# Kernel tuning notes

Measured on AMD Instinct MI355X. Metric: run time of the kernel, lower is better.

Reference implementation:

```python
import jax, jax.numpy as jnp
import numpy as np

LAMB = 0.01
DISTILL = 1.0
NUM_CLASSES = 10


def _reverse_seq(x, lens):
    # TF reverse_sequence semantics: reverse first `lens[i]` steps of row i.
    T = x.shape[1]
    t = jnp.arange(T)[None, :]
    idx = jnp.where(t < lens[:, None], lens[:, None] - 1 - t, t)
    return jnp.take_along_axis(x, idx[:, :, None], axis=1)


def _run_gru(x, lens, Wg, bg, Wc, bc):
    # TF GRUCell: r,z = sigmoid([x,h]Wg + bg); c = tanh([x, r*h]Wc + bc); h' = z*h + (1-z)*c
    # dynamic_rnn: past sequence_length, state is frozen and output is zero.
    N, T, _ = x.shape
    H = Wc.shape[1]
    h0 = jnp.zeros((N, H), x.dtype)

    def step(h, inp):
        x_t, t = inp
        xh = jnp.concatenate([x_t, h], axis=-1)
        rz = jax.nn.sigmoid(xh @ Wg + bg)
        r, z = jnp.split(rz, 2, axis=-1)
        c = jnp.tanh(jnp.concatenate([x_t, r * h], axis=-1) @ Wc + bc)
        h_new = z * h + (1.0 - z) * c
        valid = (t < lens)[:, None]
        return jnp.where(valid, h_new, h), jnp.where(valid, h_new, 0.0)

    _, outs = jax.lax.scan(step, h0, (x.transpose(1, 0, 2), jnp.arange(T)))
    return outs.transpose(1, 0, 2)  # [N, T, H]


def _bigru(x, lens, pfw, pbw):
    fw = _run_gru(x, lens, *pfw)
    bw = _reverse_seq(_run_gru(_reverse_seq(x, lens), lens, *pbw), lens)
    return jnp.concatenate([fw, bw], axis=-1)  # [N, T, 2H]


def _attention(out, Wa, ba, u):
    # additive attention: tanh projection -> score with context vector -> softmax -> weighted sum
    proj = jnp.tanh(out @ Wa + ba)                      # [N, T, A]
    score = jnp.squeeze(proj @ u, -1) / DISTILL         # [N, T]
    att = jax.nn.softmax(score, axis=1)
    vec = jnp.einsum('nt,nth->nh', att, out)            # [N, 2H]
    return vec, att


def setup_inputs() -> dict:
    key = jax.random.key(0)
    ks = jax.random.split(key, 40)
    B, D, S, E, H, C = 64, 40, 50, 200, 128, 10
    rn = lambda k, shp, s=0.1: (jax.random.normal(k, shp) * s).astype(jnp.float32)
    inp = {}
    inp['X_sentence'] = jax.random.normal(ks[0], (B, D, S, E), jnp.float32)
    inp['y'] = jax.random.randint(ks[1], (B,), 0, C).astype(jnp.int32)
    inp['sentence_length'] = jax.random.randint(ks[2], (B * D,), 1, S + 1).astype(jnp.int32)
    inp['document_length'] = jax.random.randint(ks[3], (B,), 1, D + 1).astype(jnp.int32)
    inp['dropout'] = 0
    inp['is_training'] = 0
    i = [4]
    def nxt():
        k = ks[i[0]]; i[0] += 1; return k
    for lvl, din in (('l', E), ('h', 2 * H)):
        for d in ('f', 'b'):
            inp['wg' + d + '_' + lvl] = rn(nxt(), (din + H, 2 * H))
            inp['bg' + d + '_' + lvl] = jnp.ones((2 * H,), jnp.float32)  # TF GRU gate bias init = 1.0
            inp['wc' + d + '_' + lvl] = rn(nxt(), (din + H, H))
            inp['bc' + d + '_' + lvl] = jnp.zeros((H,), jnp.float32)
        inp['wa_' + lvl] = rn(nxt(), (2 * H, H))
        inp['ba_' + lvl] = jnp.zeros((H,), jnp.float32)
    inp['uw'] = rn(nxt(), (H, 1), 1.0)  # random_normal stddev=1.0 as in source
    inp['us'] = rn(nxt(), (H, 1), 1.0)
    inp['wp'] = rn(nxt(), (2 * H, C))
    inp['bp'] = jnp.zeros((C,), jnp.float32)
    return inp


def reference(X_sentence, y, sentence_length, document_length, dropout, is_training,
              wgf_l, bgf_l, wcf_l, bcf_l, wgb_l, bgb_l, wcb_l, bcb_l, wa_l, ba_l,
              wgf_h, bgf_h, wcf_h, bcf_h, wgb_h, bgb_h, wcb_h, bcb_h, wa_h, ba_h,
              uw, us, wp, bp):
    # inference mode (is_training=False -> tf.layers.dropout is identity)
    B, D, S, E = X_sentence.shape
    x = X_sentence.reshape(B * D, S, E)
    # word level
    low = _bigru(x, sentence_length, (wgf_l, bgf_l, wcf_l, bcf_l), (wgb_l, bgb_l, wcb_l, bcb_l))
    sent_vec, att_low = _attention(low, wa_l, ba_l, uw)            # [B*D, 2H], [B*D, S]
    sent = sent_vec.reshape(B, D, -1)
    # sentence level
    high = _bigru(sent, document_length, (wgf_h, bgf_h, wcf_h, bcf_h), (wgb_h, bgb_h, wcb_h, bcb_h))
    doc_vec, att_high = _attention(high, wa_h, ba_h, us)           # [B, 2H], [B, D]
    logits = doc_vec @ wp + bp                                     # [B, C]
    logp = jax.nn.log_softmax(logits, axis=-1)
    loss = -jnp.mean(jnp.take_along_axis(logp, y[:, None], axis=1))
    # regularizer exactly as in source (note h kernel counted twice, h bias omitted)
    loss = loss + LAMB * (jnp.sum(wa_l ** 2) + jnp.sum(ba_l ** 2)
                          + 2.0 * jnp.sum(wa_h ** 2)
                          + jnp.sum(uw ** 2) + jnp.sum(us ** 2))
    predict = jnp.argmax(logits, axis=1).astype(jnp.int32)
    accuracy = jnp.mean((y == predict).astype(jnp.float32))
    return (loss, predict, accuracy, att_low, att_high)
```

## Files before the change

### kernel.cpp

```cpp
#include <hip/hip_runtime.h>
#include <hip/hip_bf16.h>


typedef __attribute__((ext_vector_type(8))) short short8;
typedef __attribute__((ext_vector_type(4))) float f32x4;

__device__ __forceinline__ float fsigmoid(float x) { return 1.f / (1.f + __expf(-x)); }
__device__ __forceinline__ float ftanh(float x)    { float e = __expf(2.f * x); return 1.f - 2.f / (e + 1.f); }

__device__ __forceinline__ unsigned short f2bf(float x) {
    unsigned int u = __builtin_bit_cast(unsigned int, x);
    u += 0x7fffu + ((u >> 16) & 1u);
    return (unsigned short)(u >> 16);
}
__device__ __forceinline__ float bf2f(unsigned short h) {
    unsigned int u = ((unsigned int)h) << 16;
    return __builtin_bit_cast(float, u);
}
__device__ __forceinline__ uint4 pack8(const unsigned short* v) {
    uint4 r;
    r.x = (unsigned int)v[0] | ((unsigned int)v[1] << 16);
    r.y = (unsigned int)v[2] | ((unsigned int)v[3] << 16);
    r.z = (unsigned int)v[4] | ((unsigned int)v[5] << 16);
    r.w = (unsigned int)v[6] | ((unsigned int)v[7] << 16);
    return r;
}
__device__ __forceinline__ void cvt8(const float* v, short8& hi, short8& lo) {
    unsigned short h[8], l[8];
#pragma unroll
    for (int j = 0; j < 8; ++j) {
        unsigned short hh = f2bf(v[j]);
        h[j] = hh;
        l[j] = f2bf(v[j] - bf2f(hh));
    }
    uint4 uh = pack8(h), ul = pack8(l);
    hi = __builtin_bit_cast(short8, uh);
    lo = __builtin_bit_cast(short8, ul);
}

__global__ __launch_bounds__(256) void pack_weights(
    const float* __restrict__ wg_f, const float* __restrict__ bg_f,
    const float* __restrict__ wc_f, const float* __restrict__ bc_f,
    const float* __restrict__ wg_b, const float* __restrict__ bg_b,
    const float* __restrict__ wc_b, const float* __restrict__ bc_b,
    float* __restrict__ W, float* __restrict__ bias, int E)
{
    int idx = blockIdx.x * 256 + threadIdx.x;
    if (idx < 768) {
        int c = idx; float v;
        if (c < 256) v = bg_f[c];
        else if (c < 384) v = bc_f[c - 256];
        else if (c < 640) v = bg_b[c - 384];
        else v = bc_b[c - 640];
        bias[c] = v;
    }
    if (idx >= E * 768) return;
    int k = idx / 768, c = idx - k * 768;
    float v;
    if (c < 256) v = wg_f[k * 256 + c];
    else if (c < 384) v = wc_f[k * 128 + (c - 256)];
    else if (c < 640) v = wg_b[k * 256 + (c - 384)];
    else v = wc_b[k * 128 + (c - 640)];
    W[idx] = v;
}

__global__ __launch_bounds__(256) void pack_a_frag(
    const float* __restrict__ src, uint4* __restrict__ dstH, uint4* __restrict__ dstL,
    int Mr16, int KC, int Ks)
{
    int idx = blockIdx.x * 256 + threadIdx.x;
    if (idx >= Mr16 * KC * 64) return;
    int lane = idx & 63;
    int g = idx >> 6;
    int mb = g / KC, kc = g - mb * KC;
    int m = lane & 15, quad = lane >> 4;
    int row = mb * 16 + m;
    int k0 = kc * 32 + quad * 8;
    const float* s = src + (size_t)row * Ks;
    unsigned short hi[8], lo[8];
#pragma unroll
    for (int j = 0; j < 8; ++j) {
        float x = (k0 + j < Ks) ? s[k0 + j] : 0.f;
        unsigned short h = f2bf(x);
        hi[j] = h;
        lo[j] = f2bf(x - bf2f(h));
    }
    dstH[idx] = pack8(hi);
    dstL[idx] = pack8(lo);
}

__global__ __launch_bounds__(256) void pack_w_frag(
    const float* __restrict__ src, uint4* __restrict__ dstH, uint4* __restrict__ dstL,
    int N16, int KC, int Ks, int N)
{
    int idx = blockIdx.x * 256 + threadIdx.x;
    if (idx >= N16 * KC * 64) return;
    int lane = idx & 63;
    int g = idx >> 6;
    int nb = g / KC, kc = g - nb * KC;
    int m = lane & 15, quad = lane >> 4;
    int n = nb * 16 + m;
    int k0 = kc * 32 + quad * 8;
    unsigned short hi[8], lo[8];
#pragma unroll
    for (int j = 0; j < 8; ++j) {
        float x = (k0 + j < Ks) ? src[(size_t)(k0 + j) * N + n] : 0.f;
        unsigned short h = f2bf(x);
        hi[j] = h;
        lo[j] = f2bf(x - bf2f(h));
    }
    dstH[idx] = pack8(hi);
    dstL[idx] = pack8(lo);
}

__global__ __launch_bounds__(256) void pack_rec(
    const float* __restrict__ wgf, const float* __restrict__ wgb,
    const float* __restrict__ wcf, const float* __restrict__ wcb,
    uint4* __restrict__ RgH, uint4* __restrict__ RgL,
    uint4* __restrict__ RcH, uint4* __restrict__ RcL)
{
    int sel = blockIdx.y;
    const float* src; uint4 *dH, *dL; int N16, N;
    if (sel == 0)      { src = wgf; dH = RgH;        dL = RgL;        N16 = 16; N = 256; }
    else if (sel == 1) { src = wgb; dH = RgH + 4096; dL = RgL + 4096; N16 = 16; N = 256; }
    else if (sel == 2) { src = wcf; dH = RcH;        dL = RcL;        N16 = 8;  N = 128; }
    else               { src = wcb; dH = RcH + 2048; dL = RcL + 2048; N16 = 8;  N = 128; }
    int idx = blockIdx.x * 256 + threadIdx.x;
    if (idx >= N16 * 4 * 64) return;
    int lane = idx & 63;
    int g = idx >> 6;
    int nb = g / 4, kc = g - nb * 4;
    int m = lane & 15, quad = lane >> 4;
    int n = nb * 16 + m;
    int k0 = kc * 32 + quad * 8;
    unsigned short hi[8], lo[8];
#pragma unroll
    for (int j = 0; j < 8; ++j) {
        float x = src[(size_t)(k0 + j) * N + n];
        unsigned short h = f2bf(x);
        hi[j] = h;
        lo[j] = f2bf(x - bf2f(h));
    }
    dH[idx] = pack8(hi);
    dL[idx] = pack8(lo);
}

__global__ __launch_bounds__(256) void mfma_gemm(
    const uint4* __restrict__ Ah, const uint4* __restrict__ Al,
    const uint4* __restrict__ Bh, const uint4* __restrict__ Bl,
    const float* __restrict__ bias, float* __restrict__ C,
    int KC, int ldc, int act)
{
    int tid = threadIdx.x;
    int lane = tid & 63;
    int w = tid >> 6;
    int wm = w >> 1, wn = w & 1;
    int quad = lane >> 4, m = lane & 15;
    int bm = blockIdx.x, bn = blockIdx.y;
    f32x4 acc[4][4];
#pragma unroll
    for (int i = 0; i < 4; ++i)
#pragma unroll
        for (int j = 0; j < 4; ++j) acc[i][j] = (f32x4){0.f, 0.f, 0.f, 0.f};

    size_t aBase[4], bBase[4];
#pragma unroll
    for (int i = 0; i < 4; ++i) {
        aBase[i] = ((size_t)(bm * 8 + wm * 4 + i) * KC) * 64 + quad * 16 + m;
        bBase[i] = ((size_t)(bn * 8 + wn * 4 + i) * KC) * 64 + quad * 16 + m;
    }
    for (int kc = 0; kc < KC; ++kc) {
        short8 ah[4], al[4], bh[4], bl[4];
#pragma unroll
        for (int i = 0; i < 4; ++i) {
            ah[i] = __builtin_bit_cast(short8, Ah[aBase[i]]);
            al[i] = __builtin_bit_cast(short8, Al[aBase[i]]);
            bh[i] = __builtin_bit_cast(short8, Bh[bBase[i]]);
            bl[i] = __builtin_bit_cast(short8, Bl[bBase[i]]);
            aBase[i] += 64; bBase[i] += 64;
        }
#pragma unroll
        for (int i = 0; i < 4; ++i)
#pragma unroll
            for (int j = 0; j < 4; ++j) {
                acc[i][j] = __builtin_amdgcn_mfma_f32_16x16x32_bf16(ah[i], bh[j], acc[i][j], 0, 0, 0);
                acc[i][j] = __builtin_amdgcn_mfma_f32_16x16x32_bf16(ah[i], bl[j], acc[i][j], 0, 0, 0);
                acc[i][j] = __builtin_amdgcn_mfma_f32_16x16x32_bf16(al[i], bh[j], acc[i][j], 0, 0, 0);
            }
    }
#pragma unroll
    for (int i = 0; i < 4; ++i) {
        int row0 = bm * 128 + wm * 64 + i * 16 + quad * 4;
#pragma unroll
        for (int j = 0; j < 4; ++j) {
            int col = bn * 128 + wn * 64 + j * 16 + m;
            float b = bias[col];
#pragma unroll
            for (int r = 0; r < 4; ++r) {
                float v = acc[i][j][r] + b;
                if (act) v = ftanh(v);
                C[(size_t)(row0 + r) * ldc + col] = v;
            }
        }
    }
}

__global__ __launch_bounds__(256) void bigru_mfma(
    const float* __restrict__ G,
    const uint4* __restrict__ WgH, const uint4* __restrict__ WgL,
    const uint4* __restrict__ WcH, const uint4* __restrict__ WcL,
    const int* __restrict__ lens,
    float* __restrict__ outbuf,
    int rowOff, int T)
{
    __shared__ float hs[16][132];
    __shared__ float zs[16][132];
    __shared__ uint4 hfH[4][64], hfL[4][64];
    __shared__ uint4 rfH[4][64], rfL[4][64];
    __shared__ int Ls[16];

    int tid = threadIdx.x;
    int dir = blockIdx.x & 1;
    int rg0 = (blockIdx.x >> 1) * 16;
    int lane = tid & 63, w = tid >> 6;
    int quad = lane >> 4, mc = lane & 15;
    for (int i = tid; i < 16 * 132; i += 256) { (&hs[0][0])[i] = 0.f; }
    for (int i = tid; i < 256; i += 256) { hfH[0][i] = (uint4){0,0,0,0}; hfL[0][i] = (uint4){0,0,0,0}; }
    if (tid < 16) Ls[tid] = lens[rowOff + rg0 + tid];
    __syncthreads();
    const int goff = dir * 384;
    unsigned short* hfHu = (unsigned short*)hfH;
    unsigned short* hfLu = (unsigned short*)hfL;
    unsigned short* rfHu = (unsigned short*)rfH;
    unsigned short* rfLu = (unsigned short*)rfL;

    for (int t = 0; t < T; ++t) {
        int Lr[4], tir[4];
#pragma unroll
        for (int r = 0; r < 4; ++r) {
            int L = Ls[quad * 4 + r];
            Lr[r] = L;
            tir[r] = dir ? ((t < L) ? (L - 1 - t) : t) : t;
        }
        float gG[4][4], gC[2][4];
#pragma unroll
        for (int r = 0; r < 4; ++r) {
            const float* gbase = &G[((size_t)(rg0 + quad * 4 + r) * T + tir[r]) * 768 + goff];
#pragma unroll
            for (int i = 0; i < 4; ++i) gG[i][r] = gbase[(w * 4 + i) * 16 + mc];
#pragma unroll
            for (int i = 0; i < 2; ++i) gC[i][r] = gbase[256 + (w * 2 + i) * 16 + mc];
        }
        f32x4 ga[4];
#pragma unroll
        for (int i = 0; i < 4; ++i) ga[i] = (f32x4){0.f, 0.f, 0.f, 0.f};
#pragma unroll
        for (int kc = 0; kc < 4; ++kc) {
            short8 ah = __builtin_bit_cast(short8, hfH[kc][lane]);
            short8 al = __builtin_bit_cast(short8, hfL[kc][lane]);
#pragma unroll
            for (int i = 0; i < 4; ++i) {
                size_t idx = (((size_t)(dir * 16 + w * 4 + i) * 4 + kc) << 6) + lane;
                short8 bh = __builtin_bit_cast(short8, WgH[idx]);
                short8 bl = __builtin_bit_cast(short8, WgL[idx]);
                ga[i] = __builtin_amdgcn_mfma_f32_16x16x32_bf16(ah, bh, ga[i], 0, 0, 0);
                ga[i] = __builtin_amdgcn_mfma_f32_16x16x32_bf16(ah, bl, ga[i], 0, 0, 0);
                ga[i] = __builtin_amdgcn_mfma_f32_16x16x32_bf16(al, bh, ga[i], 0, 0, 0);
            }
        }
#pragma unroll
        for (int i = 0; i < 4; ++i) {
            int n = (w * 4 + i) * 16 + mc;
#pragma unroll
            for (int r = 0; r < 4; ++r) {
                int m = quad * 4 + r;
                float s = fsigmoid(ga[i][r] + gG[i][r]);
                if (n < 128) {
                    float rh = s * hs[m][n];
                    unsigned short hi = f2bf(rh);
                    int fi = ((((n >> 5) * 64) + (((n >> 3) & 3) * 16) + m) << 3) + (n & 7);
                    rfHu[fi] = hi;
                    rfLu[fi] = f2bf(rh - bf2f(hi));
                } else {
                    zs[m][n - 128] = s;
                }
            }
        }
        __syncthreads();
        f32x4 ca[2];
#pragma unroll
        for (int i = 0; i < 2; ++i) ca[i] = (f32x4){0.f, 0.f, 0.f, 0.f};
#pragma unroll
        for (int kc = 0; kc < 4; ++kc) {
            short8 ar = __builtin_bit_cast(short8, rfH[kc][lane]);
            short8 al = __builtin_bit_cast(short8, rfL[kc][lane]);
#pragma unroll
            for (int i = 0; i < 2; ++i) {
                size_t idx = (((size_t)(dir * 8 + w * 2 + i) * 4 + kc) << 6) + lane;
                short8 bh = __builtin_bit_cast(short8, WcH[idx]);
                short8 bl = __builtin_bit_cast(short8, WcL[idx]);
                ca[i] = __builtin_amdgcn_mfma_f32_16x16x32_bf16(ar, bh, ca[i], 0, 0, 0);
                ca[i] = __builtin_amdgcn_mfma_f32_16x16x32_bf16(ar, bl, ca[i], 0, 0, 0);
                ca[i] = __builtin_amdgcn_mfma_f32_16x16x32_bf16(al, bh, ca[i], 0, 0, 0);
            }
        }
#pragma unroll
        for (int i = 0; i < 2; ++i) {
            int n = (w * 2 + i) * 16 + mc;
            int fi0 = ((((n >> 5) * 64) + (((n >> 3) & 3) * 16)) << 3) + (n & 7);
#pragma unroll
            for (int r = 0; r < 4; ++r) {
                int m = quad * 4 + r;
                bool valid = (t < Lr[r]);
                float cd = ftanh(ca[i][r] + gC[i][r]);
                float z = zs[m][n];
                float h = hs[m][n];
                float hn = z * h + (1.f - z) * cd;
                float ov = valid ? hn : 0.f;
                if (valid) {
                    hs[m][n] = hn;
                    unsigned short hi = f2bf(hn);
                    int fi = fi0 + (m << 3);
                    hfHu[fi] = hi;
                    hfLu[fi] = f2bf(hn - bf2f(hi));
                }
                outbuf[((size_t)(rg0 + m) * T + tir[r]) * 256 + dir * 128 + n] = ov;
            }
        }
        __syncthreads();
    }
}

__global__ __launch_bounds__(256) void attn_fused(
    const float* __restrict__ outv,
    const uint4* __restrict__ WaH, const uint4* __restrict__ WaL,
    const float* __restrict__ ba, const float* __restrict__ u,
    float* __restrict__ att_out,
    float* __restrict__ vec,
    int T, int attRowOff)
{
    __shared__ float lowS[50][260];
    __shared__ float scoreS[64];
    __shared__ float attS[64];
    int n = blockIdx.x;
    int tid = threadIdx.x;
    int lane = tid & 63, w = tid >> 6;
    int quad = lane >> 4, mc = lane & 15;

    const float4* src4 = (const float4*)(outv + (size_t)n * T * 256);
    for (int idx = tid; idx < T * 64; idx += 256) {
        int row = idx >> 6, c4 = idx & 63;
        float4 v = src4[idx];
        *(float4*)&lowS[row][c4 * 4] = v;
    }
    __syncthreads();

    f32x4 acc[8];
#pragma unroll
    for (int j = 0; j < 8; ++j) acc[j] = (f32x4){0.f, 0.f, 0.f, 0.f};
    int rowA = w * 16 + mc;
    bool rowValid = rowA < T;
#pragma unroll
    for (int kc = 0; kc < 8; ++kc) {
        float v[8];
        if (rowValid) {
            const float* p = &lowS[rowA][kc * 32 + quad * 8];
#pragma unroll
            for (int j = 0; j < 8; ++j) v[j] = p[j];
        } else {
#pragma unroll
            for (int j = 0; j < 8; ++j) v[j] = 0.f;
        }
        short8 ah, al;
        cvt8(v, ah, al);
#pragma unroll
        for (int nt = 0; nt < 8; ++nt) {
            size_t idx = (((size_t)nt * 8 + kc) << 6) + lane;
            short8 bh = __builtin_bit_cast(short8, WaH[idx]);
            short8 bl = __builtin_bit_cast(short8, WaL[idx]);
            acc[nt] = __builtin_amdgcn_mfma_f32_16x16x32_bf16(ah, bh, acc[nt], 0, 0, 0);
            acc[nt] = __builtin_amdgcn_mfma_f32_16x16x32_bf16(ah, bl, acc[nt], 0, 0, 0);
            acc[nt] = __builtin_amdgcn_mfma_f32_16x16x32_bf16(al, bh, acc[nt], 0, 0, 0);
        }
    }
    float sc[4] = {0.f, 0.f, 0.f, 0.f};
#pragma unroll
    for (int nt = 0; nt < 8; ++nt) {
        int col = nt * 16 + mc;
        float bb = ba[col], uu = u[col];
#pragma unroll
        for (int r = 0; r < 4; ++r)
            sc[r] += ftanh(acc[nt][r] + bb) * uu;
    }
#pragma unroll
    for (int off = 1; off < 16; off <<= 1) {
#pragma unroll
        for (int r = 0; r < 4; ++r) sc[r] += __shfl_xor(sc[r], off);
    }
    if (mc == 0) {
#pragma unroll
        for (int r = 0; r < 4; ++r) scoreS[w * 16 + quad * 4 + r] = sc[r];
    }
    __syncthreads();
    if (w == 0) {
        float s = (lane < T) ? scoreS[lane] : -3.402823466e38f;
        float m = s;
#pragma unroll
        for (int off = 1; off < 64; off <<= 1) m = fmaxf(m, __shfl_xor(m, off));
        float e = (lane < T) ? __expf(s - m) : 0.f;
        float sum = e;
#pragma unroll
        for (int off = 1; off < 64; off <<= 1) sum += __shfl_xor(sum, off);
        float att = e / sum;
        attS[lane] = att;
        if (lane < T) att_out[(size_t)(attRowOff + n) * T + lane] = att;
    }
    __syncthreads();
    float a = 0.f;
    for (int t = 0; t < T; ++t) a += attS[t] * lowS[t][tid];
    vec[(size_t)n * 256 + tid] = a;
}

__global__ __launch_bounds__(256) void head_kernel(
    const float* __restrict__ dvec, const float* __restrict__ wp, const float* __restrict__ bp,
    const int* __restrict__ y,
    const float* __restrict__ wa_l, const float* __restrict__ ba_l, const float* __restrict__ wa_h,
    const float* __restrict__ uw, const float* __restrict__ us,
    float* __restrict__ out)
{
    __shared__ float lg[64][10];
    __shared__ float red[256];
    int tid = threadIdx.x;
    for (int idx = tid; idx < 640; idx += 256) {
        int r = idx / 10, c = idx % 10;
        float a = bp[c];
        const float* dv = dvec + r * 256;
        for (int k = 0; k < 256; ++k) a += dv[k] * wp[k * 10 + c];
        lg[r][c] = a;
    }
    __syncthreads();
    float lossv = 0.f, corr = 0.f;
    if (tid < 64) {
        float m = lg[tid][0]; int arg = 0;
        for (int c = 1; c < 10; ++c) if (lg[tid][c] > m) { m = lg[tid][c]; arg = c; }
        float se = 0.f;
        for (int c = 0; c < 10; ++c) se += __expf(lg[tid][c] - m);
        float lse = m + __logf(se);
        int yy = y[tid];
        lossv = -(lg[tid][yy] - lse);
        corr = (yy == arg) ? 1.f : 0.f;
        out[1 + tid] = (float)arg;
    }
    float rs = 0.f;
    for (int i = tid; i < 32768; i += 256) {
        float v = wa_l[i]; rs += v * v;
        float w = wa_h[i]; rs += 2.f * w * w;
    }
    if (tid < 128) {
        float v1 = ba_l[tid], v2 = uw[tid], v3 = us[tid];
        rs += v1 * v1 + v2 * v2 + v3 * v3;
    }
    red[tid] = lossv; __syncthreads();
    for (int o = 128; o > 0; o >>= 1) { if (tid < o) red[tid] += red[tid + o]; __syncthreads(); }
    float totLoss = red[0]; __syncthreads();
    red[tid] = corr; __syncthreads();
    for (int o = 128; o > 0; o >>= 1) { if (tid < o) red[tid] += red[tid + o]; __syncthreads(); }
    float totCorr = red[0]; __syncthreads();
    red[tid] = rs; __syncthreads();
    for (int o = 128; o > 0; o >>= 1) { if (tid < o) red[tid] += red[tid + o]; __syncthreads(); }
    float totReg = red[0];
    if (tid == 0) {
        out[0] = totLoss / 64.f + 0.01f * totReg;
        out[65] = totCorr / 64.f;
    }
}

extern "C" void kernel_launch(void* const* d_in, const int* in_sizes, int n_in,
                              void* d_out, int out_size, void* d_ws, size_t ws_size,
                              hipStream_t stream)
{
    const float* X    = (const float*)d_in[0];
    const int*   y    = (const int*)d_in[1];
    const int*   slen = (const int*)d_in[2];
    const int*   dlen = (const int*)d_in[3];
    const float* wgf_l = (const float*)d_in[6];
    const float* bgf_l = (const float*)d_in[7];
    const float* wcf_l = (const float*)d_in[8];
    const float* bcf_l = (const float*)d_in[9];
    const float* wgb_l = (const float*)d_in[10];
    const float* bgb_l = (const float*)d_in[11];
    const float* wcb_l = (const float*)d_in[12];
    const float* bcb_l = (const float*)d_in[13];
    const float* wa_l  = (const float*)d_in[14];
    const float* ba_l  = (const float*)d_in[15];
    const float* wgf_h = (const float*)d_in[16];
    const float* bgf_h = (const float*)d_in[17];
    const float* wcf_h = (const float*)d_in[18];
    const float* bcf_h = (const float*)d_in[19];
    const float* wgb_h = (const float*)d_in[20];
    const float* bgb_h = (const float*)d_in[21];
    const float* wcb_h = (const float*)d_in[22];
    const float* bcb_h = (const float*)d_in[23];
    const float* wa_h  = (const float*)d_in[24];
    const float* ba_h  = (const float*)d_in[25];
    const float* uw    = (const float*)d_in[26];
    const float* us    = (const float*)d_in[27];
    const float* wp    = (const float*)d_in[28];
    const float* bp    = (const float*)d_in[29];
    float* out = (float*)d_out;

    int NCH = 1;
    while (NCH < 8) {
        size_t M1t = 128000ull / NCH;
        size_t needB = (M1t * 1248ull + 5200000ull) * 4ull;
        if (needB <= ws_size) break;
        NCH *= 2;
    }
    size_t nRows = 2560 / NCH;
    size_t M1 = nRows * 50;

    float* G1     = (float*)d_ws;
    float* low    = G1 + M1 * 768;
    float* AXf    = low + M1 * 256;
    float* sent   = AXf + M1 * 224;
    float* Gs     = sent + 655360;
    float* high   = Gs + 1966080;
    float* dvec   = high + 655360;
    float* pSf    = dvec + 16384;
    float* WpackL = pSf + 655360;
    float* biasL  = WpackL + 153600;
    float* WLf    = biasL + 768;
    float* WpackH = WLf + 172032;
    float* biasH  = WpackH + 196608;
    float* WHf    = biasH + 768;
    float* WaLf   = WHf + 196608;
    float* WaHf   = WaLf + 32768;
    float* RgLf   = WaHf + 32768;
    float* RcLf   = RgLf + 65536;
    float* RgHf   = RcLf + 32768;
    float* RcHf   = RgHf + 65536;

    uint4* AXh = (uint4*)AXf;           uint4* AXl = (uint4*)(AXf + M1 * 112);
    uint4* pSh = (uint4*)pSf;           uint4* pSl = (uint4*)(pSf + 327680);
    uint4* WLh = (uint4*)WLf;           uint4* WLl = (uint4*)(WLf + 86016);
    uint4* WHh = (uint4*)WHf;           uint4* WHl = (uint4*)(WHf + 98304);
    uint4* WaLh = (uint4*)WaLf;         uint4* WaLl = (uint4*)(WaLf + 16384);
    uint4* WaHh = (uint4*)WaHf;         uint4* WaHl = (uint4*)(WaHf + 16384);
    uint4* RgLH = (uint4*)RgLf;         uint4* RgLL = (uint4*)(RgLf + 32768);
    uint4* RcLH = (uint4*)RcLf;         uint4* RcLL = (uint4*)(RcLf + 16384);
    uint4* RgHH = (uint4*)RgHf;         uint4* RgHL = (uint4*)(RgHf + 32768);
    uint4* RcHH = (uint4*)RcHf;         uint4* RcHL = (uint4*)(RcHf + 16384);

    pack_weights<<<600, 256, 0, stream>>>(wgf_l, bgf_l, wcf_l, bcf_l, wgb_l, bgb_l, wcb_l, bcb_l,
                                          WpackL, biasL, 200);
    pack_weights<<<768, 256, 0, stream>>>(wgf_h, bgf_h, wcf_h, bcf_h, wgb_h, bgb_h, wcb_h, bcb_h,
                                          WpackH, biasH, 256);
    pack_w_frag<<<84, 256, 0, stream>>>(WpackL, WLh, WLl, 48, 7, 200, 768);
    pack_w_frag<<<96, 256, 0, stream>>>(WpackH, WHh, WHl, 48, 8, 256, 768);
    pack_w_frag<<<16, 256, 0, stream>>>(wa_l, WaLh, WaLl, 8, 8, 256, 128);
    pack_w_frag<<<16, 256, 0, stream>>>(wa_h, WaHh, WaHl, 8, 8, 256, 128);
    pack_rec<<<dim3(16, 4), 256, 0, stream>>>(wgf_l + 200 * 256, wgb_l + 200 * 256,
                                              wcf_l + 200 * 128, wcb_l + 200 * 128,
                                              RgLH, RgLL, RcLH, RcLL);
    pack_rec<<<dim3(16, 4), 256, 0, stream>>>(wgf_h + 256 * 256, wgb_h + 256 * 256,
                                              wcf_h + 256 * 128, wcb_h + 256 * 128,
                                              RgHH, RgHL, RcHH, RcHL);

    for (int c = 0; c < NCH; ++c) {
        const float* Xc = X + (size_t)c * nRows * 50 * 200;
        int Mr16 = (int)(M1 / 16);
        pack_a_frag<<<(Mr16 * 7 * 64 + 255) / 256, 256, 0, stream>>>(Xc, AXh, AXl, Mr16, 7, 200);
        mfma_gemm<<<dim3((int)(M1 / 128), 6), 256, 0, stream>>>(AXh, AXl, WLh, WLl, biasL, G1, 7, 768, 0);
        bigru_mfma<<<(int)(nRows / 16) * 2, 256, 0, stream>>>(G1, RgLH, RgLL, RcLH, RcLL,
                                                              slen, low, (int)(c * nRows), 50);
        attn_fused<<<(int)nRows, 256, 0, stream>>>(low, WaLh, WaLl, ba_l, uw,
                                                   out + 66, sent + (size_t)c * nRows * 256, 50, (int)(c * nRows));
    }
    pack_a_frag<<<(160 * 8 * 64 + 255) / 256, 256, 0, stream>>>(sent, pSh, pSl, 160, 8, 256);
    mfma_gemm<<<dim3(20, 6), 256, 0, stream>>>(pSh, pSl, WHh, WHl, biasH, Gs, 8, 768, 0);
    bigru_mfma<<<8, 256, 0, stream>>>(Gs, RgHH, RgHL, RcHH, RcHL, dlen, high, 0, 40);
    attn_fused<<<64, 256, 0, stream>>>(high, WaHh, WaHl, ba_h, us, out + 128066, dvec, 40, 0);
    head_kernel<<<1, 256, 0, stream>>>(dvec, wp, bp, y, wa_l, ba_l, wa_h, uw, us, out);
}
```

Before: 1.237 ms.

## Use two-wave GRU blocks with double-buffered LDS prefetch of gate inputs

Rewrites the recurrent GRU kernel to run with 128 threads (two waves) instead of four. Each wave now does twice the MFMA tiles, and the gate split is reassigned so wave 0 computes r and wave 1 computes z. The next timestep's precomputed gate inputs are prefetched from global memory into registers and staged into a double-buffered LDS area, which takes global-load latency off the sequential critical path. The fp32 hidden-state copy is dropped and h is rebuilt from the bf16 hi/lo split. The tradeoffs are fewer waves per block, less per-step parallelism, and a large LDS footprint that may limit occupancy.

```diff
diff --git a/kernel.cpp b/kernel.cpp
--- a/kernel.cpp
+++ b/kernel.cpp
@@ -205,7 +205,7 @@
     }
 }
 
-__global__ __launch_bounds__(256) void bigru_mfma(
+__global__ __launch_bounds__(128) void bigru_wave(
     const float* __restrict__ G,
     const uint4* __restrict__ WgH, const uint4* __restrict__ WgL,
     const uint4* __restrict__ WcH, const uint4* __restrict__ WcL,
@@ -213,54 +213,82 @@
     float* __restrict__ outbuf,
     int rowOff, int T)
 {
-    __shared__ float hs[16][132];
-    __shared__ float zs[16][132];
+    __shared__ float Gb[2][6400];
     __shared__ uint4 hfH[4][64], hfL[4][64];
     __shared__ uint4 rfH[4][64], rfL[4][64];
-    __shared__ int Ls[16];
-
-    int tid = threadIdx.x;
-    int dir = blockIdx.x & 1;
-    int rg0 = (blockIdx.x >> 1) * 16;
-    int lane = tid & 63, w = tid >> 6;
-    int quad = lane >> 4, mc = lane & 15;
-    for (int i = tid; i < 16 * 132; i += 256) { (&hs[0][0])[i] = 0.f; }
-    for (int i = tid; i < 256; i += 256) { hfH[0][i] = (uint4){0,0,0,0}; hfL[0][i] = (uint4){0,0,0,0}; }
-    if (tid < 16) Ls[tid] = lens[rowOff + rg0 + tid];
-    __syncthreads();
-    const int goff = dir * 384;
+    __shared__ float zs[16][130];
+
+    const int tid = threadIdx.x;
+    const int lane = tid & 63, w = tid >> 6;
+    const int quad = lane >> 4, mc = lane & 15;
+    const int dir = blockIdx.x & 1;
+    const int rg0 = (blockIdx.x >> 1) * 16;
+
     unsigned short* hfHu = (unsigned short*)hfH;
     unsigned short* hfLu = (unsigned short*)hfL;
     unsigned short* rfHu = (unsigned short*)rfH;
     unsigned short* rfLu = (unsigned short*)rfL;
 
+    for (int i = tid; i < 256; i += 128) {
+        hfH[0][i] = (uint4){0, 0, 0, 0};
+        hfL[0][i] = (uint4){0, 0, 0, 0};
+    }
+    int Lr[4];
+#pragma unroll
+    for (int r = 0; r < 4; ++r) Lr[r] = lens[rowOff + rg0 + quad * 4 + r];
+
+    const int k0 = w * 13;
+    const int nk = w ? 12 : 13;
+    int meta[13];
+    float4 sreg[13];
+    const char* Gblk = (const char*)(G + ((size_t)rg0 * T * 768 + dir * 384));
+#pragma unroll
+    for (int k = 0; k < 13; ++k) {
+        if (k < nk) {
+            int g = (k0 + k) * 64 + lane;
+            int m = g / 97; if (m > 15) m = 15;
+            int c4 = g - m * 97; if (c4 > 96) c4 = 96;
+            int L = lens[rowOff + rg0 + m];
+            meta[k] = (m * T * 3072 + c4 * 16) | (L << 26);
+        }
+    }
+#pragma unroll
+    for (int k = 0; k < 13; ++k) if (k < nk) {
+        int off = meta[k] & 0x03FFFFFF;
+        int L = (int)(((unsigned int)meta[k]) >> 26);
+        int sel = (dir && 0 < L) ? (L - 1) : 0;
+        sreg[k] = *(const float4*)(Gblk + (size_t)off + (size_t)sel * 3072);
+    }
+    {
+        float4* dst = (float4*)&Gb[0][0];
+#pragma unroll
+        for (int k = 0; k < 13; ++k) if (k < nk) dst[(k0 + k) * 64 + lane] = sreg[k];
+    }
+    __syncthreads();
+
     for (int t = 0; t < T; ++t) {
-        int Lr[4], tir[4];
-#pragma unroll
-        for (int r = 0; r < 4; ++r) {
-            int L = Ls[quad * 4 + r];
-            Lr[r] = L;
-            tir[r] = dir ? ((t < L) ? (L - 1 - t) : t) : t;
-        }
-        float gG[4][4], gC[2][4];
-#pragma unroll
-        for (int r = 0; r < 4; ++r) {
-            const float* gbase = &G[((size_t)(rg0 + quad * 4 + r) * T + tir[r]) * 768 + goff];
-#pragma unroll
-            for (int i = 0; i < 4; ++i) gG[i][r] = gbase[(w * 4 + i) * 16 + mc];
-#pragma unroll
-            for (int i = 0; i < 2; ++i) gC[i][r] = gbase[256 + (w * 2 + i) * 16 + mc];
-        }
-        f32x4 ga[4];
-#pragma unroll
-        for (int i = 0; i < 4; ++i) ga[i] = (f32x4){0.f, 0.f, 0.f, 0.f};
+        const int buf = t & 1;
+        const float* Gv = &Gb[buf][0];
+        if (t + 1 < T) {
+#pragma unroll
+            for (int k = 0; k < 13; ++k) if (k < nk) {
+                int off = meta[k] & 0x03FFFFFF;
+                int L = (int)(((unsigned int)meta[k]) >> 26);
+                int t1 = t + 1;
+                int sel = (dir && t1 < L) ? (L - 1 - t1) : t1;
+                sreg[k] = *(const float4*)(Gblk + (size_t)off + (size_t)sel * 3072);
+            }
+        }
+        f32x4 ga[8];
+#pragma unroll
+        for (int i = 0; i < 8; ++i) ga[i] = (f32x4){0.f, 0.f, 0.f, 0.f};
 #pragma unroll
         for (int kc = 0; kc < 4; ++kc) {
             short8 ah = __builtin_bit_cast(short8, hfH[kc][lane]);
             short8 al = __builtin_bit_cast(short8, hfL[kc][lane]);
 #pragma unroll
-            for (int i = 0; i < 4; ++i) {
-                size_t idx = (((size_t)(dir * 16 + w * 4 + i) * 4 + kc) << 6) + lane;
+            for (int i = 0; i < 8; ++i) {
+                size_t idx = (((size_t)(dir * 16 + w * 8 + i) * 4 + kc) << 6) + lane;
                 short8 bh = __builtin_bit_cast(short8, WgH[idx]);
                 short8 bl = __builtin_bit_cast(short8, WgL[idx]);
                 ga[i] = __builtin_amdgcn_mfma_f32_16x16x32_bf16(ah, bh, ga[i], 0, 0, 0);
@@ -268,35 +296,45 @@
                 ga[i] = __builtin_amdgcn_mfma_f32_16x16x32_bf16(al, bh, ga[i], 0, 0, 0);
             }
         }
-#pragma unroll
-        for (int i = 0; i < 4; ++i) {
-            int n = (w * 4 + i) * 16 + mc;
-#pragma unroll
-            for (int r = 0; r < 4; ++r) {
-                int m = quad * 4 + r;
-                float s = fsigmoid(ga[i][r] + gG[i][r]);
-                if (n < 128) {
-                    float rh = s * hs[m][n];
+        if (w == 0) {
+#pragma unroll
+            for (int i = 0; i < 8; ++i) {
+#pragma unroll
+                for (int r = 0; r < 4; ++r) {
+                    int m = quad * 4 + r;
+                    int n = i * 16 + mc;
+                    float s = fsigmoid(ga[i][r] + Gv[m * 388 + n]);
+                    int fi = (((n >> 5) * 64 + ((n >> 3) & 3) * 16 + m) << 3) + (n & 7);
+                    float h = bf2f(hfHu[fi]) + bf2f(hfLu[fi]);
+                    float rh = s * h;
                     unsigned short hi = f2bf(rh);
-                    int fi = ((((n >> 5) * 64) + (((n >> 3) & 3) * 16) + m) << 3) + (n & 7);
                     rfHu[fi] = hi;
                     rfLu[fi] = f2bf(rh - bf2f(hi));
-                } else {
-                    zs[m][n - 128] = s;
                 }
             }
+        } else {
+#pragma unroll
+            for (int i = 0; i < 8; ++i) {
+#pragma unroll
+                for (int r = 0; r < 4; ++r) {
+                    int m = quad * 4 + r;
+                    int n = i * 16 + mc;
+                    float s = fsigmoid(ga[i][r] + Gv[m * 388 + 128 + n]);
+                    zs[m][n] = s;
+                }
+            }
         }
         __syncthreads();
-        f32x4 ca[2];
-#pragma unroll
-        for (int i = 0; i < 2; ++i) ca[i] = (f32x4){0.f, 0.f, 0.f, 0.f};
+        f32x4 ca[4];
+#pragma unroll
+        for (int i = 0; i < 4; ++i) ca[i] = (f32x4){0.f, 0.f, 0.f, 0.f};
 #pragma unroll
         for (int kc = 0; kc < 4; ++kc) {
             short8 ar = __builtin_bit_cast(short8, rfH[kc][lane]);
             short8 al = __builtin_bit_cast(short8, rfL[kc][lane]);
 #pragma unroll
-            for (int i = 0; i < 2; ++i) {
-                size_t idx = (((size_t)(dir * 8 + w * 2 + i) * 4 + kc) << 6) + lane;
+            for (int i = 0; i < 4; ++i) {
+                size_t idx = (((size_t)(dir * 8 + w * 4 + i) * 4 + kc) << 6) + lane;
                 short8 bh = __builtin_bit_cast(short8, WcH[idx]);
                 short8 bl = __builtin_bit_cast(short8, WcL[idx]);
                 ca[i] = __builtin_amdgcn_mfma_f32_16x16x32_bf16(ar, bh, ca[i], 0, 0, 0);
@@ -305,27 +343,30 @@
             }
         }
 #pragma unroll
-        for (int i = 0; i < 2; ++i) {
-            int n = (w * 2 + i) * 16 + mc;
-            int fi0 = ((((n >> 5) * 64) + (((n >> 3) & 3) * 16)) << 3) + (n & 7);
+        for (int i = 0; i < 4; ++i) {
 #pragma unroll
             for (int r = 0; r < 4; ++r) {
                 int m = quad * 4 + r;
+                int cn = (w * 4 + i) * 16 + mc;
+                float cd = ftanh(ca[i][r] + Gv[m * 388 + 256 + cn]);
+                float z = zs[m][cn];
+                int fi = (((cn >> 5) * 64 + ((cn >> 3) & 3) * 16 + m) << 3) + (cn & 7);
+                float h = bf2f(hfHu[fi]) + bf2f(hfLu[fi]);
+                float hn = z * h + (1.f - z) * cd;
                 bool valid = (t < Lr[r]);
-                float cd = ftanh(ca[i][r] + gC[i][r]);
-                float z = zs[m][n];
-                float h = hs[m][n];
-                float hn = z * h + (1.f - z) * cd;
-                float ov = valid ? hn : 0.f;
+                int tir = (dir && valid) ? (Lr[r] - 1 - t) : t;
                 if (valid) {
-                    hs[m][n] = hn;
                     unsigned short hi = f2bf(hn);
-                    int fi = fi0 + (m << 3);
                     hfHu[fi] = hi;
                     hfLu[fi] = f2bf(hn - bf2f(hi));
                 }
-                outbuf[((size_t)(rg0 + m) * T + tir[r]) * 256 + dir * 128 + n] = ov;
-            }
+                outbuf[((size_t)(rg0 + m) * T + tir) * 256 + dir * 128 + cn] = valid ? hn : 0.f;
+            }
+        }
+        if (t + 1 < T) {
+            float4* dst = (float4*)&Gb[buf ^ 1][0];
+#pragma unroll
+            for (int k = 0; k < 13; ++k) if (k < nk) dst[(k0 + k) * 64 + lane] = sreg[k];
         }
         __syncthreads();
     }
@@ -571,14 +612,14 @@
         int Mr16 = (int)(M1 / 16);
         pack_a_frag<<<(Mr16 * 7 * 64 + 255) / 256, 256, 0, stream>>>(Xc, AXh, AXl, Mr16, 7, 200);
         mfma_gemm<<<dim3((int)(M1 / 128), 6), 256, 0, stream>>>(AXh, AXl, WLh, WLl, biasL, G1, 7, 768, 0);
-        bigru_mfma<<<(int)(nRows / 16) * 2, 256, 0, stream>>>(G1, RgLH, RgLL, RcLH, RcLL,
+        bigru_wave<<<(int)(nRows / 16) * 2, 128, 0, stream>>>(G1, RgLH, RgLL, RcLH, RcLL,
                                                               slen, low, (int)(c * nRows), 50);
         attn_fused<<<(int)nRows, 256, 0, stream>>>(low, WaLh, WaLl, ba_l, uw,
                                                    out + 66, sent + (size_t)c * nRows * 256, 50, (int)(c * nRows));
     }
     pack_a_frag<<<(160 * 8 * 64 + 255) / 256, 256, 0, stream>>>(sent, pSh, pSl, 160, 8, 256);
     mfma_gemm<<<dim3(20, 6), 256, 0, stream>>>(pSh, pSl, WHh, WHl, biasH, Gs, 8, 768, 0);
-    bigru_mfma<<<8, 256, 0, stream>>>(Gs, RgHH, RgHL, RcHH, RcHL, dlen, high, 0, 40);
+    bigru_wave<<<8, 128, 0, stream>>>(Gs, RgHH, RgHL, RcHH, RcHL, dlen, high, 0, 40);
     attn_fused<<<64, 256, 0, stream>>>(high, WaHh, WaHl, ba_h, us, out + 128066, dvec, 40, 0);
     head_kernel<<<1, 256, 0, stream>>>(dvec, wp, bp, y, wa_l, ba_l, wa_h, uw, us, out);
 }
```

Measured after the change: 4.077 ms. +229.6%, slower.

## Replace sentence-level MFMA GRU with per-sequence FP32 GRU kernel

Applied to the files above, without the earlier changes.

Swaps the sentence-level bidirectional GRU from an 8-block MFMA kernel, which used split bf16 hi/lo recurrent weights, to a new 128-block kernel. Each block is one wavefront handling one document and one direction, and does the recurrent matvec in FP32 by reading the weights straight from global memory. This removes the pack_rec launch for the high-level weights and spreads the serial 40-step recurrence over many more compute units. In exchange, every block rereads the recurrent weights from L2 on each step, and a single wave per block exposes memory latency.

```diff
diff --git a/kernel.cpp b/kernel.cpp
--- a/kernel.cpp
+++ b/kernel.cpp
@@ -327,6 +327,79 @@
                 outbuf[((size_t)(rg0 + m) * T + tir[r]) * 256 + dir * 128 + n] = ov;
             }
         }
+        __syncthreads();
+    }
+}
+
+__global__ __launch_bounds__(64) void sent_gru(
+    const float* __restrict__ Gs,
+    const float* __restrict__ WgF, const float* __restrict__ WcF,
+    const float* __restrict__ WgB, const float* __restrict__ WcB,
+    const int* __restrict__ dlen,
+    float* __restrict__ high)
+{
+    __shared__ float hv[128], rhv[128], zv[128];
+    int b = blockIdx.x;
+    int dir = b >> 6, n = b & 63;
+    int lane = threadIdx.x;
+    const float* Wg = dir ? WgB : WgF;
+    const float* Wc = dir ? WcB : WcF;
+    int L = dlen[n];
+    for (int i = lane; i < 128; i += 64) hv[i] = 0.f;
+    __syncthreads();
+    int j0 = lane * 4;
+    int c0 = lane * 2;
+    for (int t = 0; t < 40; ++t) {
+        bool valid = (t < L);
+        int ti = (dir && valid) ? (L - 1 - t) : t;
+        const float* Grow = &Gs[((size_t)n * 40 + ti) * 768 + dir * 384];
+        float4 acc = *(const float4*)&Grow[j0];
+        for (int k = 0; k < 128; k += 4) {
+            float4 h4 = *(const float4*)&hv[k];
+            const float* wp = &Wg[(size_t)k * 256 + j0];
+            float4 w0 = *(const float4*)(wp);
+            float4 w1 = *(const float4*)(wp + 256);
+            float4 w2 = *(const float4*)(wp + 512);
+            float4 w3 = *(const float4*)(wp + 768);
+            acc.x += h4.x * w0.x + h4.y * w1.x + h4.z * w2.x + h4.w * w3.x;
+            acc.y += h4.x * w0.y + h4.y * w1.y + h4.z * w2.y + h4.w * w3.y;
+            acc.z += h4.x * w0.z + h4.y * w1.z + h4.z * w2.z + h4.w * w3.z;
+            acc.w += h4.x * w0.w + h4.y * w1.w + h4.z * w2.w + h4.w * w3.w;
+        }
+        float4 s4;
+        s4.x = fsigmoid(acc.x); s4.y = fsigmoid(acc.y);
+        s4.z = fsigmoid(acc.z); s4.w = fsigmoid(acc.w);
+        if (lane < 32) {
+            float4 ho = *(const float4*)&hv[j0];
+            float4 p;
+            p.x = s4.x * ho.x; p.y = s4.y * ho.y; p.z = s4.z * ho.z; p.w = s4.w * ho.w;
+            *(float4*)&rhv[j0] = p;
+        } else {
+            *(float4*)&zv[j0 - 128] = s4;
+        }
+        __syncthreads();
+        float ax = Grow[256 + c0], ay = Grow[256 + c0 + 1];
+        for (int k = 0; k < 128; k += 4) {
+            float4 r4 = *(const float4*)&rhv[k];
+            const float* wp = &Wc[(size_t)k * 128 + c0];
+            float2 w0 = *(const float2*)(wp);
+            float2 w1 = *(const float2*)(wp + 128);
+            float2 w2 = *(const float2*)(wp + 256);
+            float2 w3 = *(const float2*)(wp + 384);
+            ax += r4.x * w0.x + r4.y * w1.x + r4.z * w2.x + r4.w * w3.x;
+            ay += r4.x * w0.y + r4.y * w1.y + r4.z * w2.y + r4.w * w3.y;
+        }
+        float cx = ftanh(ax), cy = ftanh(ay);
+        float z0 = zv[c0], z1 = zv[c0 + 1];
+        float h0 = hv[c0], h1 = hv[c0 + 1];
+        float hn0 = z0 * h0 + (1.f - z0) * cx;
+        float hn1 = z1 * h1 + (1.f - z1) * cy;
+        __syncthreads();
+        if (valid) { hv[c0] = hn0; hv[c0 + 1] = hn1; }
+        float2 ov;
+        ov.x = valid ? hn0 : 0.f;
+        ov.y = valid ? hn1 : 0.f;
+        *(float2*)&high[((size_t)n * 40 + ti) * 256 + dir * 128 + c0] = ov;
         __syncthreads();
     }
 }
@@ -537,8 +610,6 @@
     float* WaHf   = WaLf + 32768;
     float* RgLf   = WaHf + 32768;
     float* RcLf   = RgLf + 65536;
-    float* RgHf   = RcLf + 32768;
-    float* RcHf   = RgHf + 65536;
 
     uint4* AXh = (uint4*)AXf;           uint4* AXl = (uint4*)(AXf + M1 * 112);
     uint4* pSh = (uint4*)pSf;           uint4* pSl = (uint4*)(pSf + 327680);
@@ -548,8 +619,6 @@
     uint4* WaHh = (uint4*)WaHf;         uint4* WaHl = (uint4*)(WaHf + 16384);
     uint4* RgLH = (uint4*)RgLf;         uint4* RgLL = (uint4*)(RgLf + 32768);
     uint4* RcLH = (uint4*)RcLf;         uint4* RcLL = (uint4*)(RcLf + 16384);
-    uint4* RgHH = (uint4*)RgHf;         uint4* RgHL = (uint4*)(RgHf + 32768);
-    uint4* RcHH = (uint4*)RcHf;         uint4* RcHL = (uint4*)(RcHf + 16384);
 
     pack_weights<<<600, 256, 0, stream>>>(wgf_l, bgf_l, wcf_l, bcf_l, wgb_l, bgb_l, wcb_l, bcb_l,
                                           WpackL, biasL, 200);
@@ -562,9 +631,6 @@
     pack_rec<<<dim3(16, 4), 256, 0, stream>>>(wgf_l + 200 * 256, wgb_l + 200 * 256,
                                               wcf_l + 200 * 128, wcb_l + 200 * 128,
                                               RgLH, RgLL, RcLH, RcLL);
-    pack_rec<<<dim3(16, 4), 256, 0, stream>>>(wgf_h + 256 * 256, wgb_h + 256 * 256,
-                                              wcf_h + 256 * 128, wcb_h + 256 * 128,
-                                              RgHH, RgHL, RcHH, RcHL);
 
     for (int c = 0; c < NCH; ++c) {
         const float* Xc = X + (size_t)c * nRows * 50 * 200;
@@ -578,7 +644,8 @@
     }
     pack_a_frag<<<(160 * 8 * 64 + 255) / 256, 256, 0, stream>>>(sent, pSh, pSl, 160, 8, 256);
     mfma_gemm<<<dim3(20, 6), 256, 0, stream>>>(pSh, pSl, WHh, WHl, biasH, Gs, 8, 768, 0);
-    bigru_mfma<<<8, 256, 0, stream>>>(Gs, RgHH, RgHL, RcHH, RcHL, dlen, high, 0, 40);
+    sent_gru<<<128, 64, 0, stream>>>(Gs, wgf_h + 256 * 256, wcf_h + 256 * 128,
+                                     wgb_h + 256 * 256, wcb_h + 256 * 128, dlen, high);
     attn_fused<<<64, 256, 0, stream>>>(high, WaHh, WaHl, ba_h, us, out + 128066, dvec, 40, 0);
     head_kernel<<<1, 256, 0, stream>>>(dvec, wp, bp, y, wa_l, ba_l, wa_h, uw, us, out);
 }
```

Result: slower. 1.587 ms (+28.3%).
